# Kernel tuning notes

Hardware: AMD Instinct MI355X
Metric: run time of the kernel (lower is better)

The kernel has to match this reference:

```python
import jax, jax.numpy as jnp
import numpy as np

LN_EPS = 1e-5  # torch LayerNorm default

def _phi(x):
    # elu(x) + 1 feature map
    return jax.nn.elu(x) + 1.0

def setup_inputs() -> dict:
    key = jax.random.key(0)
    ks = jax.random.split(key, 5)
    B, N, D = 4, 8192, 1024
    s = 1.0 / np.sqrt(D)
    return {
        "H": jax.random.normal(ks[0], (B, N, D), dtype=jnp.float32),
        "W_qkv": jax.random.normal(ks[1], (3 * D, D), dtype=jnp.float32) * s,
        "b_qkv": jax.random.normal(ks[2], (3 * D,), dtype=jnp.float32) * 0.01,
        "W_proj": jax.random.normal(ks[3], (D, D), dtype=jnp.float32) * s,
        "b_proj": jax.random.normal(ks[4], (D,), dtype=jnp.float32) * 0.01,
        "gamma": jnp.ones((D,), dtype=jnp.float32),
        "beta": jnp.zeros((D,), dtype=jnp.float32),
    }

def reference(H, W_qkv, b_qkv, W_proj, b_proj, gamma, beta):
    B, N, D = H.shape
    num_heads = 16
    head_dim = D // num_heads
    residual = H
    # qkv projection: (B,N,3D)
    qkv = jnp.einsum('bnd,ed->bne', H, W_qkv) + b_qkv
    qkv = qkv.reshape(B, N, 3, num_heads, head_dim).transpose(2, 0, 3, 1, 4)
    q, k, v = qkv[0], qkv[1], qkv[2]  # each (B,h,N,d)
    q = _phi(q)
    k = _phi(k)
    # kv outer-product accumulated over nodes: (B,h,d,v)
    kv = jnp.einsum('bhnd,bhnv->bhdv', k, v)
    k1 = k.sum(axis=2)  # (B,h,d)
    qkv_out = jnp.einsum('bhnd,bhdv->bhnv', q, kv)
    qk1 = jnp.sum(q * k1[:, :, None, :], axis=-1, keepdims=True)
    out = qkv_out / jnp.clip(qk1, 1e-6, None)
    # NOTE: faithful to original -- reshape (B,h,N,d) -> (B,N,D) WITHOUT head transpose
    out = out.reshape(B, N, D)
    out = jnp.einsum('bnd,ed->bne', out, W_proj) + b_proj
    # LayerNorm over last dim
    mu = out.mean(axis=-1, keepdims=True)
    var = out.var(axis=-1, keepdims=True)
    out = (out - mu) * jax.lax.rsqrt(var + LN_EPS) * gamma + beta
    # dropout is identity at inference
    return out + residual
```

## Files before the change

kernel.cpp:

```cpp
#include <hip/hip_runtime.h>


typedef __attribute__((ext_vector_type(4))) float f32x4;
typedef __attribute__((ext_vector_type(8))) short bf16x8;

__device__ __forceinline__ unsigned short f2b(float f) {
    unsigned u = __float_as_uint(f);
    u = (u + 0x7FFFu + ((u >> 16) & 1u)) >> 16;
    return (unsigned short)u;
}
__device__ __forceinline__ float b2f(unsigned short h) {
    return __uint_as_float(((unsigned)h) << 16);
}

__device__ __forceinline__ void glds16(const void* gp, void* lp) {
    __builtin_amdgcn_global_load_lds(
        (__attribute__((address_space(1))) void*)(unsigned long long)gp,
        (__attribute__((address_space(3))) void*)(unsigned int)(unsigned long long)lp,
        16, 0, 0);
}

__global__ __launch_bounds__(256) void cvt_all(const float* __restrict__ H,
                                               const float* __restrict__ Wq,
                                               const float* __restrict__ Wp,
                                               unsigned short* __restrict__ hbf,
                                               unsigned short* __restrict__ wqb,
                                               unsigned short* __restrict__ wpb) {
    const int blk = blockIdx.x;
    const float* src; unsigned short* dst; long n4; int b0, nb;
    if (blk < 1792)      { src = H;  dst = hbf; n4 = 8388608; b0 = 0;    nb = 1792; }
    else if (blk < 1920) { src = Wq; dst = wqb; n4 = 786432;  b0 = 1792; nb = 128; }
    else                 { src = Wp; dst = wpb; n4 = 262144;  b0 = 1920; nb = 64; }
    long i = (long)(blk - b0) * 256 + threadIdx.x;
    const long stride = (long)nb * 256;
    for (; i < n4; i += stride) {
        float4 v = ((const float4*)src)[i];
        ushort4 o;
        o.x = f2b(v.x); o.y = f2b(v.y); o.z = f2b(v.z); o.w = f2b(v.w);
        ((ushort4*)dst)[i] = o;
    }
}

template<int MODE>
__global__ __launch_bounds__(512) void gemm256(const unsigned short* __restrict__ A,
                                               const unsigned short* __restrict__ B,
                                               const float* __restrict__ bias,
                                               void* __restrict__ Cout,
                                               int mb, int N, int K) {
    __shared__ unsigned short lds[2][2][256][64];
    const int tid = threadIdx.x;
    const int wid = tid >> 6, lane = tid & 63;
    const int wr = wid >> 2, wc = wid & 3;
    const int lr = lane & 15, lq = lane >> 4;
    const int cpx = (int)gridDim.x >> 3;
    const int L = ((int)blockIdx.x & 7) * cpx + ((int)blockIdx.x >> 3);
    const int bm = L % mb, bn = L / mb;
    const size_t aRow0 = (size_t)bm * 256, bRow0 = (size_t)bn * 256;

    const int sr8 = lane >> 3;
    const int ssw = ((lane & 7) ^ sr8) * 8;
    const unsigned short* aG = A + (aRow0 + (size_t)(wid * 8 + sr8)) * K + ssw;
    const unsigned short* bG = B + (bRow0 + (size_t)(wid * 8 + sr8)) * K + ssw;

    f32x4 acc[8][4] = {};
    const char* base = (const char*)&lds[0][0][0][0];

    auto stage = [&](int buf, int k0) {
#pragma unroll
        for (int j = 0; j < 8; ++j) {
            const unsigned short* g = (j < 4 ? aG : bG) + (size_t)(j & 3) * 64 * K + k0;
            glds16(g, &lds[buf][j >> 2][(j & 3) * 64 + wid * 8][0]);
        }
    };
    auto ldA = [&](int cur, int mi, int ks) {
        int row = wr * 128 + mi * 16 + lr;
        int off = (cur * 2 + 0) * 32768 + row * 128 + ((((ks << 2) | lq) ^ (row & 7)) << 4);
        return *(const bf16x8*)(base + off);
    };
    auto ldB = [&](int cur, int ni, int ks) {
        int row = wc * 64 + ni * 16 + lr;
        int off = (cur * 2 + 1) * 32768 + row * 128 + ((((ks << 2) | lq) ^ (row & 7)) << 4);
        return *(const bf16x8*)(base + off);
    };

    const int nt = K >> 6;
    stage(0, 0);
    asm volatile("s_waitcnt vmcnt(0)" ::: "memory");
    __builtin_amdgcn_s_barrier();

    bf16x8 af[4][2], bfr[4][2];
    for (int t = 0; t < nt; ++t) {
        const int cur = t & 1;
#pragma unroll
        for (int mi = 0; mi < 4; ++mi) {
            af[mi][0] = ldA(cur, mi, 0); af[mi][1] = ldA(cur, mi, 1);
        }
#pragma unroll
        for (int ni = 0; ni < 2; ++ni) {
            bfr[ni][0] = ldB(cur, ni, 0); bfr[ni][1] = ldB(cur, ni, 1);
        }
        if (t + 1 < nt) stage(cur ^ 1, (t + 1) << 6);
        __builtin_amdgcn_s_barrier();
        __builtin_amdgcn_s_setprio(1);
#pragma unroll
        for (int mi = 0; mi < 4; ++mi)
#pragma unroll
            for (int ni = 0; ni < 2; ++ni)
#pragma unroll
                for (int ks = 0; ks < 2; ++ks)
                    acc[mi][ni] = __builtin_amdgcn_mfma_f32_16x16x32_bf16(
                        af[mi][ks], bfr[ni][ks], acc[mi][ni], 0, 0, 0);
        __builtin_amdgcn_s_setprio(0);
        __builtin_amdgcn_s_barrier();
#pragma unroll
        for (int ni = 2; ni < 4; ++ni) {
            bfr[ni][0] = ldB(cur, ni, 0); bfr[ni][1] = ldB(cur, ni, 1);
        }
        __builtin_amdgcn_s_barrier();
        __builtin_amdgcn_s_setprio(1);
#pragma unroll
        for (int mi = 0; mi < 4; ++mi)
#pragma unroll
            for (int ni = 2; ni < 4; ++ni)
#pragma unroll
                for (int ks = 0; ks < 2; ++ks)
                    acc[mi][ni] = __builtin_amdgcn_mfma_f32_16x16x32_bf16(
                        af[mi][ks], bfr[ni][ks], acc[mi][ni], 0, 0, 0);
        __builtin_amdgcn_s_setprio(0);
        __builtin_amdgcn_s_barrier();
#pragma unroll
        for (int mi = 0; mi < 4; ++mi) {
            af[mi][0] = ldA(cur, mi + 4, 0); af[mi][1] = ldA(cur, mi + 4, 1);
        }
        __builtin_amdgcn_s_barrier();
        __builtin_amdgcn_s_setprio(1);
#pragma unroll
        for (int mi = 0; mi < 4; ++mi)
#pragma unroll
            for (int ni = 2; ni < 4; ++ni)
#pragma unroll
                for (int ks = 0; ks < 2; ++ks)
                    acc[mi + 4][ni] = __builtin_amdgcn_mfma_f32_16x16x32_bf16(
                        af[mi][ks], bfr[ni][ks], acc[mi + 4][ni], 0, 0, 0);
        __builtin_amdgcn_s_setprio(0);
        __builtin_amdgcn_s_barrier();
        __builtin_amdgcn_s_setprio(1);
#pragma unroll
        for (int mi = 0; mi < 4; ++mi)
#pragma unroll
            for (int ni = 0; ni < 2; ++ni)
#pragma unroll
                for (int ks = 0; ks < 2; ++ks)
                    acc[mi + 4][ni] = __builtin_amdgcn_mfma_f32_16x16x32_bf16(
                        af[mi][ks], bfr[ni][ks], acc[mi + 4][ni], 0, 0, 0);
        __builtin_amdgcn_s_setprio(0);
        asm volatile("s_waitcnt vmcnt(0)" ::: "memory");
        __builtin_amdgcn_s_barrier();
        __builtin_amdgcn_sched_barrier(0);
    }
#pragma unroll
    for (int mi = 0; mi < 8; ++mi) {
#pragma unroll
        for (int ni = 0; ni < 4; ++ni) {
            int col = (int)bRow0 + wc * 64 + ni * 16 + lr;
            float bv = bias[col];
#pragma unroll
            for (int r = 0; r < 4; ++r) {
                size_t row = aRow0 + wr * 128 + mi * 16 + lq * 4 + r;
                float v = acc[mi][ni][r] + bv;
                if (MODE == 0) {
                    if (col < 2048) v = (v > 0.f) ? (v + 1.f) : __expf(v);
                }
                ((unsigned short*)Cout)[row * (size_t)N + col] = f2b(v);
            }
        }
    }
}

__global__ __launch_bounds__(256) void kv_partial(const unsigned short* __restrict__ qkv,
                                                  float* __restrict__ part) {
    const int bh = blockIdx.x, chunk = blockIdx.y;
    const int b = bh >> 4, h = bh & 15;
    __shared__ unsigned short kb[16][64];
    __shared__ unsigned short vb[16][64];
    const int tid = threadIdx.x;
    const int d0 = (tid >> 4) * 4, v0 = (tid & 15) * 4;
    float acc[4][4] = {};
    float k1a[4] = {0.f, 0.f, 0.f, 0.f};
    const size_t base = ((size_t)b * 8192 + (size_t)chunk * 1024) * 3072;
    const int nn = tid >> 4;
    const int which = (tid >> 3) & 1;
    const int cg = tid & 7;
    const size_t loff = base + (size_t)nn * 3072 + (which ? 2048 : 1024) + h * 64 + cg * 8;

    for (int n0 = 0; n0 < 1024; n0 += 16) {
        uint4 val = *(const uint4*)(qkv + loff + (size_t)n0 * 3072);
        if (which) *(uint4*)(&vb[nn][cg * 8]) = val;
        else       *(uint4*)(&kb[nn][cg * 8]) = val;
        __syncthreads();
#pragma unroll 4
        for (int j = 0; j < 16; ++j) {
            ushort4 ku = *(const ushort4*)(&kb[j][d0]);
            ushort4 vu = *(const ushort4*)(&vb[j][v0]);
            float kd[4] = {b2f(ku.x), b2f(ku.y), b2f(ku.z), b2f(ku.w)};
            float vd[4] = {b2f(vu.x), b2f(vu.y), b2f(vu.z), b2f(vu.w)};
#pragma unroll
            for (int i = 0; i < 4; ++i)
#pragma unroll
                for (int jj = 0; jj < 4; ++jj)
                    acc[i][jj] += kd[i] * vd[jj];
            if ((tid & 15) == 0)
#pragma unroll
                for (int i = 0; i < 4; ++i) k1a[i] += kd[i];
        }
        __syncthreads();
    }
    float* dst = part + ((size_t)bh * 8 + chunk) * 4160;
#pragma unroll
    for (int i = 0; i < 4; ++i)
#pragma unroll
        for (int jj = 0; jj < 4; ++jj)
            dst[(d0 + i) * 64 + v0 + jj] = acc[i][jj];
    if ((tid & 15) == 0)
#pragma unroll
        for (int i = 0; i < 4; ++i) dst[4096 + d0 + i] = k1a[i];
}

__global__ __launch_bounds__(256) void kv_reduce(const float* __restrict__ part,
                                                 float* __restrict__ kvk1) {
    const int bh = blockIdx.x;
    for (int idx = threadIdx.x; idx < 4160; idx += 256) {
        float s = 0.f;
#pragma unroll
        for (int c = 0; c < 8; ++c) s += part[((size_t)bh * 8 + c) * 4160 + idx];
        kvk1[(size_t)bh * 4160 + idx] = s;
    }
}

__global__ __launch_bounds__(256) void apply_attn(const unsigned short* __restrict__ qkv,
                                                  const float* __restrict__ kvk1,
                                                  unsigned short* __restrict__ att) {
    const int nblk = blockIdx.x;
    const int bh = blockIdx.y;
    const int b = bh >> 4, h = bh & 15;
    __shared__ float kvs[64][64];
    __shared__ float k1s[64];
    const float* src = kvk1 + (size_t)bh * 4160;
    for (int i = threadIdx.x; i < 4096; i += 256) kvs[i >> 6][i & 63] = src[i];
    if (threadIdx.x < 64) k1s[threadIdx.x] = src[4096 + threadIdx.x];
    __syncthreads();
    const int t = threadIdx.x;
    const int r = t >> 2, qt = t & 3;
    const int n = nblk * 64 + r;
    const unsigned short* qrow = qkv + ((size_t)b * 8192 + n) * 3072 + h * 64;
    float acc[16] = {};
    float qk1 = 0.f;
    for (int dc = 0; dc < 64; dc += 8) {
        uint4 qu = *(const uint4*)(qrow + dc);
        unsigned qw[4] = {qu.x, qu.y, qu.z, qu.w};
#pragma unroll
        for (int jj = 0; jj < 8; ++jj) {
            float qd = (jj & 1) ? __uint_as_float(qw[jj >> 1] & 0xFFFF0000u)
                                : __uint_as_float(qw[jj >> 1] << 16);
            int d = dc + jj;
            qk1 += qd * k1s[d];
            const float4* kr = (const float4*)(&kvs[d][qt * 16]);
            float4 c0 = kr[0], c1 = kr[1], c2 = kr[2], c3 = kr[3];
            acc[0]  += qd * c0.x; acc[1]  += qd * c0.y; acc[2]  += qd * c0.z; acc[3]  += qd * c0.w;
            acc[4]  += qd * c1.x; acc[5]  += qd * c1.y; acc[6]  += qd * c1.z; acc[7]  += qd * c1.w;
            acc[8]  += qd * c2.x; acc[9]  += qd * c2.y; acc[10] += qd * c2.z; acc[11] += qd * c2.w;
            acc[12] += qd * c3.x; acc[13] += qd * c3.y; acc[14] += qd * c3.z; acc[15] += qd * c3.w;
        }
    }
    float rinv = 1.f / fmaxf(qk1, 1e-6f);
    union { unsigned short us[16]; uint4 u4[2]; } ob;
#pragma unroll
    for (int j = 0; j < 16; ++j) ob.us[j] = f2b(acc[j] * rinv);
    unsigned short* dst = att + (((size_t)b * 8192) + h * 512 + (n >> 4)) * 1024
                              + (n & 15) * 64 + qt * 16;
    *(uint4*)dst = ob.u4[0];
    *(uint4*)(dst + 8) = ob.u4[1];
}

__global__ __launch_bounds__(256) void ln_residual(const unsigned short* __restrict__ X,
                                                   const float* __restrict__ H,
                                                   const float* __restrict__ gamma,
                                                   const float* __restrict__ beta,
                                                   float* __restrict__ out,
                                                   int nrows) {
    const int lane = threadIdx.x & 63;
    int row = blockIdx.x * 4 + (threadIdx.x >> 6);
    const int rstride = gridDim.x * 4;
    for (; row < nrows; row += rstride) {
        const unsigned short* x = X + (size_t)row * 1024;
        float v[16];
        float s = 0.f, s2 = 0.f;
#pragma unroll
        for (int j = 0; j < 4; ++j) {
            ushort4 u = *(const ushort4*)(x + j * 256 + lane * 4);
            float a = b2f(u.x), b = b2f(u.y), c = b2f(u.z), d = b2f(u.w);
            v[j * 4 + 0] = a; v[j * 4 + 1] = b; v[j * 4 + 2] = c; v[j * 4 + 3] = d;
            s += a + b + c + d;
            s2 += a * a + b * b + c * c + d * d;
        }
#pragma unroll
        for (int o = 32; o > 0; o >>= 1) {
            s  += __shfl_xor(s, o, 64);
            s2 += __shfl_xor(s2, o, 64);
        }
        const float mu = s * (1.f / 1024.f);
        const float var = s2 * (1.f / 1024.f) - mu * mu;
        const float inv = rsqrtf(var + 1e-5f);
        const float* hrow = H + (size_t)row * 1024;
        float* orow = out + (size_t)row * 1024;
#pragma unroll
        for (int j = 0; j < 4; ++j) {
            const int c = j * 256 + lane * 4;
            float4 g = *(const float4*)(gamma + c);
            float4 bt = *(const float4*)(beta + c);
            float4 hr = *(const float4*)(hrow + c);
            float4 o;
            o.x = (v[j * 4 + 0] - mu) * inv * g.x + bt.x + hr.x;
            o.y = (v[j * 4 + 1] - mu) * inv * g.y + bt.y + hr.y;
            o.z = (v[j * 4 + 2] - mu) * inv * g.z + bt.z + hr.z;
            o.w = (v[j * 4 + 3] - mu) * inv * g.w + bt.w + hr.w;
            *(float4*)(orow + c) = o;
        }
    }
}

extern "C" void kernel_launch(void* const* d_in, const int* in_sizes, int n_in,
                              void* d_out, int out_size, void* d_ws, size_t ws_size,
                              hipStream_t stream) {
    const float* H     = (const float*)d_in[0];
    const float* Wqkv  = (const float*)d_in[1];
    const float* bqkv  = (const float*)d_in[2];
    const float* Wproj = (const float*)d_in[3];
    const float* bproj = (const float*)d_in[4];
    const float* gamma = (const float*)d_in[5];
    const float* beta  = (const float*)d_in[6];
    float* out = (float*)d_out;
    char* ws = (char*)d_ws;

    unsigned short* wq_bf = (unsigned short*)(ws);
    unsigned short* wp_bf = (unsigned short*)(ws + 6291456);
    unsigned short* hbf   = (unsigned short*)(ws + 8388608);
    unsigned short* att   = hbf;
    unsigned short* qkvbf = (unsigned short*)(ws + 75497472);
    unsigned short* out2  = (unsigned short*)(ws + 75497472);
    float*          kvk1  = (float*)(ws + 276824064);
    float*          part  = (float*)(ws + 277889024);

    cvt_all<<<1984, 256, 0, stream>>>(H, Wqkv, Wproj, hbf, wq_bf, wp_bf);

    gemm256<0><<<1536, 512, 0, stream>>>(hbf, wq_bf, bqkv, (void*)qkvbf,
                                         128, 3072, 1024);

    kv_partial<<<dim3(64, 8), 256, 0, stream>>>(qkvbf, part);
    kv_reduce<<<64, 256, 0, stream>>>(part, kvk1);

    apply_attn<<<dim3(128, 64), 256, 0, stream>>>(qkvbf, kvk1, att);

    gemm256<1><<<512, 512, 0, stream>>>(att, wp_bf, bproj, (void*)out2,
                                        128, 1024, 1024);

    ln_residual<<<2048, 256, 0, stream>>>(out2, H, gamma, beta, out, 32768);
}
```

Baseline: 605.4 us.

## Fold kv reduction into apply_attn and use 128x128 tile GEMM for projection

Removes the separate kv_reduce launch by having each apply_attn block sum the 8 partial kv/k1 chunks directly while loading into shared memory. Adds a new 128x128-tile, 256-thread GEMM with double-buffered LDS staging, and uses it for the output projection in place of the 256-tile kernel, giving 2048 blocks instead of 512 for better occupancy across CUs. The trade-off is redundant reduction reads (each of 128 blocks per head re-sums the partials) and lower per-block data reuse in the smaller GEMM tile.

```diff
diff --git a/kernel.cpp b/kernel.cpp
--- a/kernel.cpp
+++ b/kernel.cpp
@@ -177,6 +177,95 @@
     }
 }
 
+template<int MODE>
+__global__ __launch_bounds__(256, 2) void gemm128(const unsigned short* __restrict__ A,
+                                                  const unsigned short* __restrict__ B,
+                                                  const float* __restrict__ bias,
+                                                  void* __restrict__ Cout,
+                                                  int mb, int N, int K) {
+    __shared__ unsigned short lds[2][2][128][64];
+    const int tid = threadIdx.x;
+    const int wave = tid >> 6, lane = tid & 63;
+    const int wr = wave >> 1, wc = wave & 1;
+    const int lr = lane & 15, lq = lane >> 4;
+    const int cpx = (int)gridDim.x >> 3;
+    const int L = ((int)blockIdx.x & 7) * cpx + ((int)blockIdx.x >> 3);
+    const int bm = L % mb, bn = L / mb;
+    const size_t aRow0 = (size_t)bm * 128, bRow0 = (size_t)bn * 128;
+
+    const int sr8 = lane >> 3;
+    const int ssw = ((lane & 7) ^ sr8) * 8;
+    const unsigned short* aG = A + (aRow0 + (size_t)(wave * 32 + sr8)) * K + ssw;
+    const unsigned short* bG = B + (bRow0 + (size_t)(wave * 32 + sr8)) * K + ssw;
+
+    f32x4 acc[4][4] = {};
+    const char* base = (const char*)&lds[0][0][0][0];
+
+    auto stage = [&](int buf, int k0) {
+#pragma unroll
+        for (int i = 0; i < 4; ++i) {
+            glds16(aG + (size_t)i * 8 * K + k0, &lds[buf][0][wave * 32 + i * 8][0]);
+            glds16(bG + (size_t)i * 8 * K + k0, &lds[buf][1][wave * 32 + i * 8][0]);
+        }
+    };
+
+    const int nt = K >> 6;
+    stage(0, 0);
+    for (int t = 0; t < nt; ++t) {
+        const int cur = t & 1;
+        if (t + 1 < nt) {
+            stage(cur ^ 1, (t + 1) << 6);
+            asm volatile("s_waitcnt vmcnt(8)" ::: "memory");
+        } else {
+            asm volatile("s_waitcnt vmcnt(0)" ::: "memory");
+        }
+        __builtin_amdgcn_s_barrier();
+        bf16x8 af[4][2], bfr[4][2];
+#pragma unroll
+        for (int mi = 0; mi < 4; ++mi)
+#pragma unroll
+            for (int ks = 0; ks < 2; ++ks) {
+                int row = wr * 64 + mi * 16 + lr;
+                af[mi][ks] = *(const bf16x8*)(base + (cur * 2 + 0) * 16384 + row * 128
+                                              + ((((ks << 2) | lq) ^ (row & 7)) << 4));
+            }
+#pragma unroll
+        for (int ni = 0; ni < 4; ++ni)
+#pragma unroll
+            for (int ks = 0; ks < 2; ++ks) {
+                int row = wc * 64 + ni * 16 + lr;
+                bfr[ni][ks] = *(const bf16x8*)(base + (cur * 2 + 1) * 16384 + row * 128
+                                               + ((((ks << 2) | lq) ^ (row & 7)) << 4));
+            }
+#pragma unroll
+        for (int ks = 0; ks < 2; ++ks)
+#pragma unroll
+            for (int mi = 0; mi < 4; ++mi)
+#pragma unroll
+                for (int ni = 0; ni < 4; ++ni)
+                    acc[mi][ni] = __builtin_amdgcn_mfma_f32_16x16x32_bf16(
+                        af[mi][ks], bfr[ni][ks], acc[mi][ni], 0, 0, 0);
+        __builtin_amdgcn_s_barrier();
+    }
+#pragma unroll
+    for (int mi = 0; mi < 4; ++mi) {
+#pragma unroll
+        for (int ni = 0; ni < 4; ++ni) {
+            int col = (int)bRow0 + wc * 64 + ni * 16 + lr;
+            float bv = bias[col];
+#pragma unroll
+            for (int r = 0; r < 4; ++r) {
+                size_t row = aRow0 + wr * 64 + mi * 16 + lq * 4 + r;
+                float v = acc[mi][ni][r] + bv;
+                if (MODE == 0) {
+                    if (col < 2048) v = (v > 0.f) ? (v + 1.f) : __expf(v);
+                }
+                ((unsigned short*)Cout)[row * (size_t)N + col] = f2b(v);
+            }
+        }
+    }
+}
+
 __global__ __launch_bounds__(256) void kv_partial(const unsigned short* __restrict__ qkv,
                                                   float* __restrict__ part) {
     const int bh = blockIdx.x, chunk = blockIdx.y;
@@ -226,28 +315,27 @@
         for (int i = 0; i < 4; ++i) dst[4096 + d0 + i] = k1a[i];
 }
 
-__global__ __launch_bounds__(256) void kv_reduce(const float* __restrict__ part,
-                                                 float* __restrict__ kvk1) {
-    const int bh = blockIdx.x;
-    for (int idx = threadIdx.x; idx < 4160; idx += 256) {
-        float s = 0.f;
-#pragma unroll
-        for (int c = 0; c < 8; ++c) s += part[((size_t)bh * 8 + c) * 4160 + idx];
-        kvk1[(size_t)bh * 4160 + idx] = s;
-    }
-}
-
 __global__ __launch_bounds__(256) void apply_attn(const unsigned short* __restrict__ qkv,
-                                                  const float* __restrict__ kvk1,
+                                                  const float* __restrict__ part,
                                                   unsigned short* __restrict__ att) {
     const int nblk = blockIdx.x;
     const int bh = blockIdx.y;
     const int b = bh >> 4, h = bh & 15;
     __shared__ float kvs[64][64];
     __shared__ float k1s[64];
-    const float* src = kvk1 + (size_t)bh * 4160;
-    for (int i = threadIdx.x; i < 4096; i += 256) kvs[i >> 6][i & 63] = src[i];
-    if (threadIdx.x < 64) k1s[threadIdx.x] = src[4096 + threadIdx.x];
+    const float* src = part + (size_t)bh * 8 * 4160;
+    for (int i = threadIdx.x; i < 4096; i += 256) {
+        float s = 0.f;
+#pragma unroll
+        for (int c = 0; c < 8; ++c) s += src[c * 4160 + i];
+        kvs[i >> 6][i & 63] = s;
+    }
+    if (threadIdx.x < 64) {
+        float s = 0.f;
+#pragma unroll
+        for (int c = 0; c < 8; ++c) s += src[c * 4160 + 4096 + threadIdx.x];
+        k1s[threadIdx.x] = s;
+    }
     __syncthreads();
     const int t = threadIdx.x;
     const int r = t >> 2, qt = t & 3;
@@ -348,7 +436,6 @@
     unsigned short* att   = hbf;
     unsigned short* qkvbf = (unsigned short*)(ws + 75497472);
     unsigned short* out2  = (unsigned short*)(ws + 75497472);
-    float*          kvk1  = (float*)(ws + 276824064);
     float*          part  = (float*)(ws + 277889024);
 
     cvt_all<<<1984, 256, 0, stream>>>(H, Wqkv, Wproj, hbf, wq_bf, wp_bf);
@@ -357,12 +444,11 @@
                                          128, 3072, 1024);
 
     kv_partial<<<dim3(64, 8), 256, 0, stream>>>(qkvbf, part);
-    kv_reduce<<<64, 256, 0, stream>>>(part, kvk1);
-
-    apply_attn<<<dim3(128, 64), 256, 0, stream>>>(qkvbf, kvk1, att);
-
-    gemm256<1><<<512, 512, 0, stream>>>(att, wp_bf, bproj, (void*)out2,
-                                        128, 1024, 1024);
+
+    apply_attn<<<dim3(128, 64), 256, 0, stream>>>(qkvbf, part, att);
+
+    gemm128<1><<<2048, 256, 0, stream>>>(att, wp_bf, bproj, (void*)out2,
+                                         256, 1024, 1024);
 
     ln_residual<<<2048, 256, 0, stream>>>(out2, H, gamma, beta, out, 32768);
 }
```

New measurement: 633.9 us. 1.05x slower.
